# Kernel tuning notes

Hardware: AMD Instinct MI355X
Metric: run time of the kernel (lower is better)

Reference implementation:

```python
import jax, jax.numpy as jnp
import numpy as np

N, E = 100000, 800000
D_IN, D_HID, D_OUT = 128, 128, 40


def _lin_params(key, d_out, d_in, bias):
    k1, k2 = jax.random.split(key)
    bound = 1.0 / np.sqrt(d_in)
    W = jax.random.uniform(k1, (d_out, d_in), jnp.float32, -bound, bound)
    if bias:
        b = jax.random.uniform(k2, (d_out,), jnp.float32, -bound, bound)
        return W, b
    return W


def setup_inputs() -> dict:
    key = jax.random.key(0)
    ks = jax.random.split(key, 8)
    x = jax.random.normal(ks[0], (N, D_IN), jnp.float32)
    edge_index = jax.random.randint(ks[1], (2, E), 0, N, jnp.int64)
    Wl0, b0 = _lin_params(ks[2], D_HID, D_IN, True)
    Wr0 = _lin_params(ks[3], D_HID, D_IN, False)
    Wl1, b1 = _lin_params(ks[4], D_HID, D_HID, True)
    Wr1 = _lin_params(ks[5], D_HID, D_HID, False)
    Wl2, b2 = _lin_params(ks[6], D_OUT, D_HID, True)
    Wr2 = _lin_params(ks[7], D_OUT, D_HID, False)
    return {"x": x, "edge_index": edge_index,
            "Wl0": Wl0, "Wr0": Wr0, "b0": b0,
            "Wl1": Wl1, "Wr1": Wr1, "b1": b1,
            "Wl2": Wl2, "Wr2": Wr2, "b2": b2}


def _sage_conv(x, src, dst, Wl, Wr, b):
    # mean aggregation of neighbor messages (src -> dst), PyG SAGEConv semantics
    msg = x[src]                                               # [E, d]
    agg = jax.ops.segment_sum(msg, dst, num_segments=N)        # [N, d]
    deg = jax.ops.segment_sum(jnp.ones((src.shape[0],), x.dtype), dst,
                              num_segments=N)                  # [N]
    agg = agg / jnp.maximum(deg, 1.0)[:, None]
    # out = lin_l(agg) + lin_r(x); lin_l has bias, lin_r does not
    return agg @ Wl.T + x @ Wr.T + b


def reference(x, edge_index, Wl0, Wr0, b0, Wl1, Wr1, b1, Wl2, Wr2, b2):
    src, dst = edge_index[0], edge_index[1]
    h = jax.nn.relu(_sage_conv(x, src, dst, Wl0, Wr0, b0))   # dropout = identity in eval
    h = jax.nn.relu(_sage_conv(h, src, dst, Wl1, Wr1, b1))
    h = _sage_conv(h, src, dst, Wl2, Wr2, b2)
    return jax.nn.log_softmax(h, axis=1)
```

## Files before the change

kernel.cpp:

```cpp
#include <hip/hip_runtime.h>
#include <hip/hip_bf16.h>
#include <math.h>

#define D 128
typedef unsigned int uint;
typedef unsigned short ushort;

using bf16x8 = __attribute__((ext_vector_type(8))) short;
using f32x4  = __attribute__((ext_vector_type(4))) float;
using f32x2  = __attribute__((ext_vector_type(2))) float;

static __device__ __forceinline__ ushort f2b(float f) {
    __hip_bfloat16 h = __float2bfloat16(f);
    return __builtin_bit_cast(ushort, h);
}
static __device__ __forceinline__ float blo(uint u) {
    uint v = u << 16;
    return __builtin_bit_cast(float, v);
}
static __device__ __forceinline__ float bhi(uint u) {
    uint v = u & 0xFFFF0000u;
    return __builtin_bit_cast(float, v);
}

__global__ void k_degpos(const int* __restrict__ dst, int* __restrict__ deg,
                         int* __restrict__ pos, int E) {
    int e = blockIdx.x * 256 + threadIdx.x;
    if (e < E) pos[e] = atomicAdd(&deg[dst[e]], 1);
}

__global__ void k_scan1(const int* __restrict__ deg, int* __restrict__ rowptr,
                        int* __restrict__ bsum, int nN) {
    __shared__ int s[256];
    int tid = threadIdx.x;
    int i = blockIdx.x * 256 + tid;
    int v = (i < nN) ? deg[i] : 0;
    s[tid] = v;
    __syncthreads();
#pragma unroll
    for (int o = 1; o < 256; o <<= 1) {
        int t = (tid >= o) ? s[tid - o] : 0;
        __syncthreads();
        s[tid] += t;
        __syncthreads();
    }
    if (i < nN) rowptr[i] = s[tid] - v;
    if (tid == 255) bsum[blockIdx.x] = s[255];
}

__global__ void k_scan2(int* __restrict__ bsum, int nb) {
    __shared__ int s[512];
    __shared__ int carry_s;
    int tid = threadIdx.x;
    if (tid == 0) carry_s = 0;
    __syncthreads();
    for (int base = 0; base < nb; base += 512) {
        int i = base + tid;
        int v = (i < nb) ? bsum[i] : 0;
        s[tid] = v;
        __syncthreads();
#pragma unroll
        for (int o = 1; o < 512; o <<= 1) {
            int t = (tid >= o) ? s[tid - o] : 0;
            __syncthreads();
            s[tid] += t;
            __syncthreads();
        }
        int carry = carry_s;
        if (i < nb) bsum[i] = s[tid] - v + carry;
        int total = s[511];
        __syncthreads();
        if (tid == 0) carry_s = carry + total;
        __syncthreads();
    }
}

__global__ void k_scan3(int* __restrict__ rowptr, const int* __restrict__ bsum,
                        int nN, int E) {
    int i = blockIdx.x * 256 + threadIdx.x;
    if (i < nN) rowptr[i] = rowptr[i] + bsum[blockIdx.x];
    if (i == 0) rowptr[nN] = E;
}

__global__ void k_place2(const int* __restrict__ src, const int* __restrict__ dst,
                         const int* __restrict__ rowptr, const int* __restrict__ pos,
                         int* __restrict__ col, int E) {
    int e = blockIdx.x * 256 + threadIdx.x;
    if (e < E) col[rowptr[dst[e]] + pos[e]] = src[e];
}

__global__ void k_cast(const float* __restrict__ x, ushort* __restrict__ Abuf, int n4) {
    int i = blockIdx.x * 256 + threadIdx.x;
    if (i >= n4) return;
    float4 v = *(const float4*)(x + (size_t)i * 4);
    int node = i >> 5;
    int coff = (i & 31) * 4;
    ushort4 o;
    o.x = f2b(v.x); o.y = f2b(v.y); o.z = f2b(v.z); o.w = f2b(v.w);
    *(ushort4*)(Abuf + (size_t)node * 256 + 128 + coff) = o;
}

__global__ void k_prepw(const float* __restrict__ Wl0, const float* __restrict__ Wr0,
                        const float* __restrict__ Wl1, const float* __restrict__ Wr1,
                        const float* __restrict__ Wl2, const float* __restrict__ Wr2,
                        ushort* __restrict__ Wtg0, ushort* __restrict__ Wtg1,
                        ushort* __restrict__ W2tg) {
    int idx = blockIdx.x * 256 + threadIdx.x;
    if (idx < 2 * 128 * 256) {
        int which = idx >> 15;
        int o = idx & 32767;
        int j = o >> 8, k = o & 255;
        const float* Wl = which ? Wl1 : Wl0;
        const float* Wr = which ? Wr1 : Wr0;
        float v = (k < 128) ? Wl[j * 128 + k] : Wr[j * 128 + (k - 128)];
        (which ? Wtg1 : Wtg0)[o] = f2b(v);
    } else {
        int o = idx - 2 * 128 * 256;
        if (o >= 80 * 128) return;
        int j = o >> 7, k = o & 127;
        float v = (j < 40) ? Wl2[j * 128 + k] : Wr2[(j - 40) * 128 + k];
        W2tg[o] = f2b(v);
    }
}

__global__ __launch_bounds__(256) void k_gather128(
    const ushort* __restrict__ feat, ushort* __restrict__ agg,
    const int* __restrict__ rowptr, const int* __restrict__ col, int nN)
{
    int node = blockIdx.x * 4 + (threadIdx.x >> 6);
    if (node >= nN) return;
    int lane = threadIdx.x & 63;
    int g = lane >> 4;
    int r = lane & 15;
    int beg = rowptr[node], end = rowptr[node + 1];
    const char* fb = (const char*)feat;
    const uint rb = (uint)(r << 4);
    float a[8];
#pragma unroll
    for (int i = 0; i < 8; ++i) a[i] = 0.f;

    int j = beg + g;
    for (; j + 4 < end; j += 8) {
        int s0 = col[j], s1 = col[j + 4];
        uint4 v0 = *(const uint4*)(fb + (((uint)s0 << 9) + rb));
        uint4 v1 = *(const uint4*)(fb + (((uint)s1 << 9) + rb));
        const uint* p0 = (const uint*)&v0;
        const uint* p1 = (const uint*)&v1;
#pragma unroll
        for (int i = 0; i < 4; ++i) {
            a[2 * i]     += blo(p0[i]) + blo(p1[i]);
            a[2 * i + 1] += bhi(p0[i]) + bhi(p1[i]);
        }
    }
    if (j < end) {
        int s0 = col[j];
        uint4 v0 = *(const uint4*)(fb + (((uint)s0 << 9) + rb));
        const uint* p0 = (const uint*)&v0;
#pragma unroll
        for (int i = 0; i < 4; ++i) {
            a[2 * i]     += blo(p0[i]);
            a[2 * i + 1] += bhi(p0[i]);
        }
    }
#pragma unroll
    for (int i = 0; i < 8; ++i) {
        a[i] += __shfl_xor(a[i], 16);
        a[i] += __shfl_xor(a[i], 32);
    }
    if (g == 0) {
        float inv = 1.0f / (float)max(end - beg, 1);
        uint4 o;
        uint* po = (uint*)&o;
#pragma unroll
        for (int i = 0; i < 4; ++i)
            po[i] = (uint)f2b(a[2 * i] * inv) | ((uint)f2b(a[2 * i + 1] * inv) << 16);
        *(uint4*)(agg + (size_t)node * 256 + r * 8) = o;
    }
}

template<int OUTJ, int KDIM, int SW, int MODE>
__global__ __launch_bounds__(256) void k_gemm_mfma(
    const ushort* __restrict__ A, int astride,
    const ushort* __restrict__ Wt, const float* __restrict__ bias,
    ushort* __restrict__ out, int ostride, ushort* __restrict__ out2, int nN)
{
    constexpr int NT = OUTJ / 16;
    constexpr int KSTEPS = KDIM / 32;
    __shared__ __align__(16) ushort Ws[OUTJ * SW];

    const int tid = threadIdx.x;
    constexpr int CHUNKS = OUTJ * KDIM / 8;
#pragma unroll
    for (int c = tid; c < CHUNKS; c += 256) {
        int row = c / (KDIM / 8);
        int ko  = (c % (KDIM / 8)) * 8;
        *(uint4*)(Ws + row * SW + ko) = *(const uint4*)(Wt + row * KDIM + ko);
    }
    __syncthreads();

    const int l = tid & 63, wv = tid >> 6;
    const int q = l >> 4, r = l & 15;
    const long long m0 = (long long)blockIdx.x * 128 + wv * 32;
    const int mA = (int)min(m0 + r, (long long)(nN - 1));
    const int mB = (int)min(m0 + 16 + r, (long long)(nN - 1));
    const ushort* pa = A + (size_t)mA * astride + q * 8;
    const ushort* pb = A + (size_t)mB * astride + q * 8;

    f32x4 acc[2][NT];
#pragma unroll
    for (int mt = 0; mt < 2; ++mt)
#pragma unroll
        for (int nt = 0; nt < NT; ++nt)
            acc[mt][nt] = (f32x4){0.f, 0.f, 0.f, 0.f};

    bf16x8 a0 = *(const bf16x8*)pa;
    bf16x8 a1 = *(const bf16x8*)pb;
#pragma unroll
    for (int ks = 0; ks < KSTEPS; ++ks) {
        bf16x8 a0n = a0, a1n = a1;
        if (ks + 1 < KSTEPS) {
            a0n = *(const bf16x8*)(pa + (ks + 1) * 32);
            a1n = *(const bf16x8*)(pb + (ks + 1) * 32);
        }
#pragma unroll
        for (int nt = 0; nt < NT; ++nt) {
            bf16x8 b = *(const bf16x8*)(Ws + (nt * 16 + r) * SW + ks * 32 + q * 8);
            acc[0][nt] = __builtin_amdgcn_mfma_f32_16x16x32_bf16(a0, b, acc[0][nt], 0, 0, 0);
            acc[1][nt] = __builtin_amdgcn_mfma_f32_16x16x32_bf16(a1, b, acc[1][nt], 0, 0, 0);
        }
        a0 = a0n; a1 = a1n;
    }

#pragma unroll
    for (int mt = 0; mt < 2; ++mt) {
#pragma unroll
        for (int i = 0; i < 4; ++i) {
            long long m = m0 + mt * 16 + q * 4 + i;
            if (m >= nN) continue;
#pragma unroll
            for (int nt = 0; nt < NT; ++nt) {
                int cc = nt * 16 + r;
                float v = acc[mt][nt][i];
                if (MODE == 0) {
                    v += bias[cc];
                    v = fmaxf(v, 0.f);
                    out[(size_t)m * ostride + cc] = f2b(v);
                } else {
                    if (cc < 40) out[(size_t)m * 40 + cc] = f2b(v);
                    else { v += bias[cc - 40]; out2[(size_t)m * 40 + (cc - 40)] = f2b(v); }
                }
            }
        }
    }
}

__global__ __launch_bounds__(256) void k_gather40_lsm(
    const ushort* __restrict__ P, const ushort* __restrict__ R,
    const int* __restrict__ rowptr, const int* __restrict__ col,
    float* __restrict__ out, int nN)
{
    int node = blockIdx.x * 4 + (threadIdx.x >> 6);
    if (node >= nN) return;
    int lane = threadIdx.x & 63;
    int g = lane >> 3;
    int r = lane & 7;
    int beg = rowptr[node], end = rowptr[node + 1];
    const char* pbase = (const char*)P;
    const uint rb = (uint)(r << 4);
    f32x2 a2[4];
#pragma unroll
    for (int i = 0; i < 4; ++i) a2[i] = (f32x2){0.f, 0.f};

    for (int j = beg + g; j < end; j += 8) {
        int s = col[j];
        uint off = (((uint)s * 5u) << 4) + rb;
        uint4 v = *(const uint4*)(pbase + off);
        const uint* p = (const uint*)&v;
#pragma unroll
        for (int i = 0; i < 4; ++i)
            a2[i] += (f32x2){blo(p[i]), bhi(p[i])};
    }
    float a[8];
#pragma unroll
    for (int i = 0; i < 4; ++i) { a[2 * i] = a2[i].x; a[2 * i + 1] = a2[i].y; }
#pragma unroll
    for (int i = 0; i < 8; ++i) {
        a[i] += __shfl_xor(a[i], 8);
        a[i] += __shfl_xor(a[i], 16);
        a[i] += __shfl_xor(a[i], 32);
    }
    float inv = 1.0f / (float)max(end - beg, 1);
    uint4 rv = *(const uint4*)(R + (size_t)node * 40 + r * 8);
    const uint* pr = (const uint*)&rv;
    float vv[8];
    float mx = -INFINITY;
#pragma unroll
    for (int i = 0; i < 8; ++i) {
        float rc = (i & 1) ? bhi(pr[i >> 1]) : blo(pr[i >> 1]);
        int c = r * 8 + i;
        vv[i] = (c < 40) ? (a[i] * inv + rc) : -INFINITY;
        mx = fmaxf(mx, vv[i]);
    }
    mx = fmaxf(mx, __shfl_xor(mx, 1));
    mx = fmaxf(mx, __shfl_xor(mx, 2));
    mx = fmaxf(mx, __shfl_xor(mx, 4));
    float s = 0.f;
#pragma unroll
    for (int i = 0; i < 8; ++i) {
        int c = r * 8 + i;
        if (c < 40) s += __expf(vv[i] - mx);
    }
    s += __shfl_xor(s, 1);
    s += __shfl_xor(s, 2);
    s += __shfl_xor(s, 4);
    float lse = mx + __logf(s);
    if (g == 0 && r < 5) {
        float4 o0 = make_float4(vv[0] - lse, vv[1] - lse, vv[2] - lse, vv[3] - lse);
        float4 o1 = make_float4(vv[4] - lse, vv[5] - lse, vv[6] - lse, vv[7] - lse);
        *(float4*)(out + (size_t)node * 40 + r * 8)     = o0;
        *(float4*)(out + (size_t)node * 40 + r * 8 + 4) = o1;
    }
}

extern "C" void kernel_launch(void* const* d_in, const int* in_sizes, int n_in,
                              void* d_out, int out_size, void* d_ws, size_t ws_size,
                              hipStream_t stream) {
    const float* x   = (const float*)d_in[0];
    const int*   ei  = (const int*)d_in[1];
    const float* Wl0 = (const float*)d_in[2];
    const float* Wr0 = (const float*)d_in[3];
    const float* b0  = (const float*)d_in[4];
    const float* Wl1 = (const float*)d_in[5];
    const float* Wr1 = (const float*)d_in[6];
    const float* b1  = (const float*)d_in[7];
    const float* Wl2 = (const float*)d_in[8];
    const float* Wr2 = (const float*)d_in[9];
    const float* b2  = (const float*)d_in[10];
    const int nN = in_sizes[0] / D;
    const int E  = in_sizes[1] / 2;
    const int* src = ei;
    const int* dst = ei + E;

    char* w = (char*)d_ws;
    auto alloc = [&](size_t bytes) { char* p = w; w += (bytes + 255) & ~(size_t)255; return p; };
    int*    deg    = (int*)   alloc((size_t)nN * 4);
    int*    rowptr = (int*)   alloc((size_t)(nN + 1) * 4);
    int*    bsum   = (int*)   alloc((size_t)((nN + 255) / 256) * 4);
    int*    col    = (int*)   alloc((size_t)E * 4);
    ushort* AbufA  = (ushort*)alloc((size_t)nN * 256 * 2);
    ushort* AbufB  = (ushort*)alloc((size_t)nN * 256 * 2);
    ushort* Wtg0   = (ushort*)alloc((size_t)128 * 256 * 2);
    ushort* Wtg1   = (ushort*)alloc((size_t)128 * 256 * 2);
    ushort* W2tg   = (ushort*)alloc((size_t)80 * 128 * 2);
    int*    pos    = (int*)AbufB;
    ushort* Pbuf   = AbufB;
    ushort* Rbuf   = AbufB + (size_t)nN * 40;
    float*  logits = (float*)d_out;

    const int NB        = (nN + 255) / 256;
    const int GATH_BLKS = (nN + 3) / 4;
    const int GEMM_BLKS = (nN + 127) / 128;
    const int PREPW_TOT = 2 * 128 * 256 + 80 * 128;

    hipMemsetAsync(deg, 0, (size_t)nN * 4, stream);
    k_degpos<<<(E + 255) / 256, 256, 0, stream>>>(dst, deg, pos, E);
    k_scan1 <<<NB, 256, 0, stream>>>(deg, rowptr, bsum, nN);
    k_scan2 <<<1, 512, 0, stream>>>(bsum, NB);
    k_scan3 <<<NB, 256, 0, stream>>>(rowptr, bsum, nN, E);
    k_place2<<<(E + 255) / 256, 256, 0, stream>>>(src, dst, rowptr, pos, col, E);
    k_cast  <<<(nN * 32 + 255) / 256, 256, 0, stream>>>(x, AbufA, nN * 32);
    k_prepw <<<(PREPW_TOT + 255) / 256, 256, 0, stream>>>(
        Wl0, Wr0, Wl1, Wr1, Wl2, Wr2, Wtg0, Wtg1, W2tg);

    k_gather128<<<GATH_BLKS, 256, 0, stream>>>(AbufA + 128, AbufA, rowptr, col, nN);
    k_gemm_mfma<128, 256, 264, 0><<<GEMM_BLKS, 256, 0, stream>>>(
        AbufA, 256, Wtg0, b0, AbufB + 128, 256, nullptr, nN);

    k_gather128<<<GATH_BLKS, 256, 0, stream>>>(AbufB + 128, AbufB, rowptr, col, nN);
    k_gemm_mfma<128, 256, 264, 0><<<GEMM_BLKS, 256, 0, stream>>>(
        AbufB, 256, Wtg1, b1, AbufA + 128, 256, nullptr, nN);

    k_gemm_mfma<80, 128, 136, 1><<<GEMM_BLKS, 256, 0, stream>>>(
        AbufA + 128, 256, W2tg, b2, Pbuf, 40, Rbuf, nN);
    k_gather40_lsm<<<GATH_BLKS, 256, 0, stream>>>(Pbuf, Rbuf, rowptr, col, logits, nN);
}
```

Measured before the change: 352.1 us.

## Map two nodes per wavefront in gather kernels and unroll 40-wide gather

```diff
diff --git a/kernel.cpp b/kernel.cpp
--- a/kernel.cpp
+++ b/kernel.cpp
@@ -127,10 +127,12 @@
     const ushort* __restrict__ feat, ushort* __restrict__ agg,
     const int* __restrict__ rowptr, const int* __restrict__ col, int nN)
 {
-    int node = blockIdx.x * 4 + (threadIdx.x >> 6);
+    int tid = threadIdx.x;
+    int lane = tid & 63;
+    int h = lane >> 5;
+    int node = blockIdx.x * 8 + ((tid >> 6) << 1) + h;
     if (node >= nN) return;
-    int lane = threadIdx.x & 63;
-    int g = lane >> 4;
+    int g = (lane >> 4) & 1;
     int r = lane & 15;
     int beg = rowptr[node], end = rowptr[node + 1];
     const char* fb = (const char*)feat;
@@ -140,8 +142,8 @@
     for (int i = 0; i < 8; ++i) a[i] = 0.f;
 
     int j = beg + g;
-    for (; j + 4 < end; j += 8) {
-        int s0 = col[j], s1 = col[j + 4];
+    for (; j + 2 < end; j += 4) {
+        int s0 = col[j], s1 = col[j + 2];
         uint4 v0 = *(const uint4*)(fb + (((uint)s0 << 9) + rb));
         uint4 v1 = *(const uint4*)(fb + (((uint)s1 << 9) + rb));
         const uint* p0 = (const uint*)&v0;
@@ -163,10 +165,8 @@
         }
     }
 #pragma unroll
-    for (int i = 0; i < 8; ++i) {
+    for (int i = 0; i < 8; ++i)
         a[i] += __shfl_xor(a[i], 16);
-        a[i] += __shfl_xor(a[i], 32);
-    }
     if (g == 0) {
         float inv = 1.0f / (float)max(end - beg, 1);
         uint4 o;
@@ -259,10 +259,12 @@
     const int* __restrict__ rowptr, const int* __restrict__ col,
     float* __restrict__ out, int nN)
 {
-    int node = blockIdx.x * 4 + (threadIdx.x >> 6);
+    int tid = threadIdx.x;
+    int lane = tid & 63;
+    int h = lane >> 5;
+    int node = blockIdx.x * 8 + ((tid >> 6) << 1) + h;
     if (node >= nN) return;
-    int lane = threadIdx.x & 63;
-    int g = lane >> 3;
+    int g = (lane >> 3) & 3;
     int r = lane & 7;
     int beg = rowptr[node], end = rowptr[node + 1];
     const char* pbase = (const char*)P;
@@ -271,14 +273,24 @@
 #pragma unroll
     for (int i = 0; i < 4; ++i) a2[i] = (f32x2){0.f, 0.f};
 
-    for (int j = beg + g; j < end; j += 8) {
-        int s = col[j];
-        uint off = (((uint)s * 5u) << 4) + rb;
-        uint4 v = *(const uint4*)(pbase + off);
-        const uint* p = (const uint*)&v;
+    int j = beg + g;
+    for (; j + 4 < end; j += 8) {
+        int s0 = col[j], s1 = col[j + 4];
+        uint4 v0 = *(const uint4*)(pbase + ((((uint)s0 * 5u) << 4) + rb));
+        uint4 v1 = *(const uint4*)(pbase + ((((uint)s1 * 5u) << 4) + rb));
+        const uint* p0 = (const uint*)&v0;
+        const uint* p1 = (const uint*)&v1;
 #pragma unroll
         for (int i = 0; i < 4; ++i)
-            a2[i] += (f32x2){blo(p[i]), bhi(p[i])};
+            a2[i] += (f32x2){blo(p0[i]) + blo(p1[i]), bhi(p0[i]) + bhi(p1[i])};
+    }
+    if (j < end) {
+        int s0 = col[j];
+        uint4 v0 = *(const uint4*)(pbase + ((((uint)s0 * 5u) << 4) + rb));
+        const uint* p0 = (const uint*)&v0;
+#pragma unroll
+        for (int i = 0; i < 4; ++i)
+            a2[i] += (f32x2){blo(p0[i]), bhi(p0[i])};
     }
     float a[8];
 #pragma unroll
@@ -287,7 +299,6 @@
     for (int i = 0; i < 8; ++i) {
         a[i] += __shfl_xor(a[i], 8);
         a[i] += __shfl_xor(a[i], 16);
-        a[i] += __shfl_xor(a[i], 32);
     }
     float inv = 1.0f / (float)max(end - beg, 1);
     uint4 rv = *(const uint4*)(R + (size_t)node * 40 + r * 8);
@@ -358,7 +369,7 @@
     float*  logits = (float*)d_out;
 
     const int NB        = (nN + 255) / 256;
-    const int GATH_BLKS = (nN + 3) / 4;
+    const int GATH_BLKS = (nN + 7) / 8;
     const int GEMM_BLKS = (nN + 127) / 128;
     const int PREPW_TOT = 2 * 128 * 256 + 80 * 128;
 
```

New measurement: 328.4 us. 1.07x faster.
